# Performance work log

Measured on AMD Instinct MI355X. Metric: run time of the kernel, lower is better.

Reference implementation:

```python
import jax, jax.numpy as jnp
import numpy as np

NUM_KEYS = 64

def setup_inputs() -> dict:
    key = jax.random.key(0)
    k1, k2 = jax.random.split(key)
    inputs = jax.random.randint(k1, (8, 4096, 1024), 0, NUM_KEYS, dtype=jnp.int32)
    # learned per-key bias (build() creates shape (num_keys,) for key_shape=[1])
    b = jax.random.normal(k2, (NUM_KEYS,), dtype=jnp.float32)
    # keys are sorted unique scalars (0..63), stored as float like the TF cast
    keys = jnp.arange(NUM_KEYS, dtype=jnp.float32)
    return {"inputs": inputs, "b": b, "keys": keys}


def reference(inputs, b, keys):
    # Original math: out = sum_k (inputs == keys[k]) * b[k], elementwise over inputs.
    # With unique sorted keys this is a gather: find the matching key index per
    # element and pick b there; elements matching no key contribute 0.
    # This avoids the O(num_keys * numel) broadcast blow-up of the TF graph.
    xf = inputs.astype(jnp.float32)
    K = keys.shape[0]
    idx = jnp.clip(jnp.searchsorted(keys, xf), 0, K - 1)  # [8,4096,1024]
    out = jnp.where(keys[idx] == xf, b[idx], jnp.float32(0.0))
    return out
```

## Files before the change

### kernel.cpp

```cpp
#include <hip/hip_runtime.h>

#define NKEYS 64

__global__ __launch_bounds__(256) void sel_xform_kernel(
    const int4* __restrict__ in,
    const float* __restrict__ b,
    const float* __restrict__ keys,
    float4* __restrict__ out,
    int nvec, int ntail, const int* __restrict__ in_tail, float* __restrict__ out_tail)
{
    __shared__ float t[NKEYS];
    const int tid = threadIdx.x;
    if (tid < NKEYS) t[tid] = 0.0f;
    __syncthreads();
    if (tid < NKEYS) {
        const float kv = keys[tid];
        const int iv = (int)kv;
        if ((float)iv == kv && iv >= 0 && iv < NKEYS) {
            t[iv] = b[tid];
        }
    }
    __syncthreads();

    int i = blockIdx.x * blockDim.x + tid;
    const int stride = gridDim.x * blockDim.x;
    for (; i < nvec; i += stride) {
        const int4 v = in[i];
        float4 o;
        o.x = ((unsigned)v.x < NKEYS) ? t[v.x] : 0.0f;
        o.y = ((unsigned)v.y < NKEYS) ? t[v.y] : 0.0f;
        o.z = ((unsigned)v.z < NKEYS) ? t[v.z] : 0.0f;
        o.w = ((unsigned)v.w < NKEYS) ? t[v.w] : 0.0f;
        out[i] = o;
    }

    if (blockIdx.x == 0 && tid < ntail) {
        const int v = in_tail[tid];
        out_tail[tid] = ((unsigned)v < NKEYS) ? t[v] : 0.0f;
    }
}

extern "C" void kernel_launch(void* const* d_in, const int* in_sizes, int n_in,
                              void* d_out, int out_size, void* d_ws, size_t ws_size,
                              hipStream_t stream) {
    const int*   x    = (const int*)d_in[0];
    const float* b    = (const float*)d_in[1];
    const float* keys = (const float*)d_in[2];
    float* out = (float*)d_out;

    const int n    = in_sizes[0];
    const int nvec = n >> 2;
    const int ntail = n & 3;

    const int block = 256;
    int grid = (nvec + block - 1) / block;
    if (grid < 1) grid = 1;

    sel_xform_kernel<<<grid, block, 0, stream>>>(
        (const int4*)x, b, keys, (float4*)out,
        nvec, ntail, x + (nvec << 2), out + (nvec << 2));
}
```

Measured before the change: 225.2 us.

## Replace shared-memory LUT with per-wave bpermute lookup and 4 vectors per thread

Each wavefront now builds its own 64-entry lookup table in registers with a bpermute-based binary search over the keys, and resolves each element with ds_bpermute instead of a shared-memory table. This removes the shared-memory initialization and the two block barriers. Each thread also handles four int4 vectors, with all loads issued before the lookup so memory latency overlaps the table build. The cost is more per-wave setup work and a fixed grid mapping; the kernel is memory-bound, so any gain is likely small.

```diff
diff --git a/kernel.cpp b/kernel.cpp
--- a/kernel.cpp
+++ b/kernel.cpp
@@ -1,42 +1,75 @@
 #include <hip/hip_runtime.h>
 
 #define NKEYS 64
+
+typedef float vfloat4 __attribute__((ext_vector_type(4)));
+
+__device__ __forceinline__ float bperm_f(int lane_idx, int src_i) {
+    return __int_as_float(__builtin_amdgcn_ds_bpermute(lane_idx << 2, src_i));
+}
 
 __global__ __launch_bounds__(256) void sel_xform_kernel(
     const int4* __restrict__ in,
     const float* __restrict__ b,
     const float* __restrict__ keys,
-    float4* __restrict__ out,
+    float* __restrict__ out,
     int nvec, int ntail, const int* __restrict__ in_tail, float* __restrict__ out_tail)
 {
-    __shared__ float t[NKEYS];
-    const int tid = threadIdx.x;
-    if (tid < NKEYS) t[tid] = 0.0f;
-    __syncthreads();
-    if (tid < NKEYS) {
-        const float kv = keys[tid];
-        const int iv = (int)kv;
-        if ((float)iv == kv && iv >= 0 && iv < NKEYS) {
-            t[iv] = b[tid];
-        }
+    const int tid  = threadIdx.x;
+    const int lane = tid & 63;
+
+    const float kv = keys[lane];
+    const float bv = b[lane];
+
+    const int i0 = blockIdx.x * 1024 + tid;
+    const int i1 = i0 + 256, i2 = i0 + 512, i3 = i0 + 768;
+    const bool p0 = i0 < nvec, p1 = i1 < nvec, p2 = i2 < nvec, p3 = i3 < nvec;
+    int4 v0{}, v1{}, v2{}, v3{};
+    if (p0) v0 = in[i0];
+    if (p1) v1 = in[i1];
+    if (p2) v2 = in[i2];
+    if (p3) v3 = in[i3];
+
+    const int   kv_i   = __float_as_int(kv);
+    const float target = (float)lane;
+    int pos = 0;
+    #pragma unroll
+    for (int s = 32; s >= 1; s >>= 1) {
+        const float kc = bperm_f(pos + s - 1, kv_i);
+        if (kc < target) pos += s;
     }
-    __syncthreads();
+    const int posc = (pos > NKEYS - 1) ? (NKEYS - 1) : pos;
+    const float kmatch = bperm_f(posc, kv_i);
+    const float bval   = bperm_f(posc, __float_as_int(bv));
+    const int tv_i = (kmatch == target) ? __float_as_int(bval) : 0;
 
-    int i = blockIdx.x * blockDim.x + tid;
-    const int stride = gridDim.x * blockDim.x;
-    for (; i < nvec; i += stride) {
-        const int4 v = in[i];
-        float4 o;
-        o.x = ((unsigned)v.x < NKEYS) ? t[v.x] : 0.0f;
-        o.y = ((unsigned)v.y < NKEYS) ? t[v.y] : 0.0f;
-        o.z = ((unsigned)v.z < NKEYS) ? t[v.z] : 0.0f;
-        o.w = ((unsigned)v.w < NKEYS) ? t[v.w] : 0.0f;
-        out[i] = o;
+    auto lut = [&](int x) -> float {
+        const float r = __int_as_float(__builtin_amdgcn_ds_bpermute(x << 2, tv_i));
+        return ((unsigned)x < NKEYS) ? r : 0.0f;
+    };
+
+    if (p0) {
+        vfloat4 o = { lut(v0.x), lut(v0.y), lut(v0.z), lut(v0.w) };
+        *(vfloat4*)(out + ((long)i0 << 2)) = o;
+    }
+    if (p1) {
+        vfloat4 o = { lut(v1.x), lut(v1.y), lut(v1.z), lut(v1.w) };
+        *(vfloat4*)(out + ((long)i1 << 2)) = o;
+    }
+    if (p2) {
+        vfloat4 o = { lut(v2.x), lut(v2.y), lut(v2.z), lut(v2.w) };
+        *(vfloat4*)(out + ((long)i2 << 2)) = o;
+    }
+    if (p3) {
+        vfloat4 o = { lut(v3.x), lut(v3.y), lut(v3.z), lut(v3.w) };
+        *(vfloat4*)(out + ((long)i3 << 2)) = o;
     }
 
     if (blockIdx.x == 0 && tid < ntail) {
-        const int v = in_tail[tid];
-        out_tail[tid] = ((unsigned)v < NKEYS) ? t[v] : 0.0f;
+        const float xf = (float)in_tail[tid];
+        float r = 0.0f;
+        for (int k = 0; k < NKEYS; ++k) r = (keys[k] == xf) ? b[k] : r;
+        out_tail[tid] = r;
     }
 }
 
@@ -48,15 +81,14 @@
     const float* keys = (const float*)d_in[2];
     float* out = (float*)d_out;
 
-    const int n    = in_sizes[0];
-    const int nvec = n >> 2;
+    const int n     = in_sizes[0];
+    const int nvec  = n >> 2;
     const int ntail = n & 3;
 
-    const int block = 256;
-    int grid = (nvec + block - 1) / block;
+    int grid = (nvec + 1023) / 1024;
     if (grid < 1) grid = 1;
 
-    sel_xform_kernel<<<grid, block, 0, stream>>>(
-        (const int4*)x, b, keys, (float4*)out,
+    sel_xform_kernel<<<grid, 256, 0, stream>>>(
+        (const int4*)x, b, keys, out,
         nvec, ntail, x + (nvec << 2), out + (nvec << 2));
 }
```

After: 229.1 us. About the same (+1.7%).
